# Kernel tuning notes

Measured on AMD Instinct MI355X. Metric: run time of the kernel, lower is better.

Reference implementation:

```python
import jax, jax.numpy as jnp
import numpy as np

NEG = -1e30  # safe -inf surrogate for log-space DP
BLANK = 0    # torch.nn.CTCLoss default blank index


def _ctc_loss_sum(lp, labels, in_lens, lab_lens):
    """CTC negative log-likelihood, summed over batch.
    lp: [T, B, V] log-probabilities; labels: [B, L] int; in_lens, lab_lens: [B] int.
    """
    T, B, V = lp.shape
    L = labels.shape[1]
    S = 2 * L + 1  # extended label length (blanks interleaved)
    s = jnp.arange(S)
    # extended label sequence z: blank at even positions, label at odd
    ext = jnp.where(s % 2 == 0, BLANK, labels[:, jnp.clip((s - 1) // 2, 0, L - 1)])  # [B,S]
    ext_m2 = jnp.concatenate([jnp.full((B, 2), BLANK, ext.dtype), ext[:, :-2]], axis=1)
    skip = (s >= 2) & (ext != BLANK) & (ext != ext_m2)  # [B,S] skip-transition allowed
    # emission log-probs gathered at extended labels: [T,B,S]
    emit = jnp.take_along_axis(lp, jnp.broadcast_to(ext[None], (T, B, S)), axis=2)
    alpha0 = jnp.full((B, S), NEG, lp.dtype)
    alpha0 = alpha0.at[:, 0].set(emit[0, :, 0]).at[:, 1].set(emit[0, :, 1])

    def step(alpha, inputs):
        emit_t, t = inputs
        a1 = jnp.concatenate([jnp.full((B, 1), NEG, alpha.dtype), alpha[:, :-1]], axis=1)
        a2 = jnp.concatenate([jnp.full((B, 2), NEG, alpha.dtype), alpha[:, :-2]], axis=1)
        comb = jnp.logaddexp(alpha, a1)
        comb = jnp.where(skip, jnp.logaddexp(comb, a2), comb)
        new = comb + emit_t
        # past each sequence's length, freeze alpha
        new = jnp.where(t < in_lens[:, None], new, alpha)
        return new, None

    alpha, _ = jax.lax.scan(step, alpha0, (emit[1:], jnp.arange(1, T)))
    s_last = 2 * lab_lens  # final blank position per sample
    bidx = jnp.arange(B)
    ll = jnp.logaddexp(alpha[bidx, s_last], alpha[bidx, s_last - 1])
    return jnp.sum(-ll)


def setup_inputs() -> dict:
    key = jax.random.key(0)
    k1, k2, k3, k4, k5, k6 = jax.random.split(key, 6)
    B, T, H, V, L = 16, 512, 512, 4096, 64
    hs_pad = jax.random.normal(k1, (B, T, H), dtype=jnp.float32)
    hs_lens = jax.random.randint(k2, (B,), T // 2, T + 1, dtype=jnp.int32)
    ys_pad = jax.random.randint(k3, (B, L), 1, V, dtype=jnp.int32)  # avoid blank=0
    ys_lens = jax.random.randint(k4, (B,), L // 2, L + 1, dtype=jnp.int32)
    W = jax.random.normal(k5, (H, V), dtype=jnp.float32) * (H ** -0.5)
    b = jax.random.normal(k6, (V,), dtype=jnp.float32) * 0.01
    return {"hs_pad": hs_pad, "hs_lens": hs_lens, "ys_pad": ys_pad,
            "ys_lens": ys_lens, "W": W, "b": b}


def reference(hs_pad, hs_lens, ys_pad, ys_lens, W, b):
    # projection (dropout_rate=0.0 -> identity) + log_softmax
    logits = jnp.einsum('bth,hv->btv', hs_pad, W) + b
    log_probs = jax.nn.log_softmax(logits, axis=-1)
    lp = jnp.transpose(log_probs, (1, 0, 2))  # [T,B,V]
    B = lp.shape[1]
    loss = _ctc_loss_sum(lp, ys_pad, hs_lens, ys_lens)
    return loss / B
```

## Files before the change

kernel.cpp:

```cpp
#include <hip/hip_runtime.h>
#include <hip/hip_bf16.h>
#include <math.h>

#define BB   16
#define TT   512
#define HH   512
#define VV   4096
#define LL   64
#define SS   129
#define JJ   65
#define MM   (BB*TT)

#define LOG2E 1.4426950408889634f
#define LN2   0.6931471805599453f

typedef __bf16 bf16;
typedef __attribute__((ext_vector_type(4))) __bf16 bf16x4;
typedef __attribute__((ext_vector_type(8))) __bf16 bf16x8;
typedef __attribute__((ext_vector_type(4))) float f32x4;

__global__ __launch_bounds__(256) void conv_hs(const float* __restrict__ hs,
                                               bf16* __restrict__ Abf)
{
    int idx = blockIdx.x * blockDim.x + threadIdx.x;
    const int n4 = MM * HH / 4;
    if (idx >= n4) return;
    float4 v = ((const float4*)hs)[idx];
    bf16x4 o = {(bf16)v.x, (bf16)v.y, (bf16)v.z, (bf16)v.w};
    *(bf16x4*)(Abf + (size_t)idx * 4) = o;
}

__global__ __launch_bounds__(256) void transpose_w(const float* __restrict__ W,
                                                   bf16* __restrict__ Wt)
{
    __shared__ float t[64][65];
    const int n0 = blockIdx.x * 64;
    const int k0 = blockIdx.y * 64;
    const int tid = threadIdx.x;
    #pragma unroll
    for (int i = 0; i < 16; ++i) {
        int idx = tid + i * 256;
        int kk = idx >> 6, nn = idx & 63;
        t[kk][nn] = W[(size_t)(k0 + kk) * VV + n0 + nn];
    }
    __syncthreads();
    #pragma unroll
    for (int i = 0; i < 16; ++i) {
        int idx = tid + i * 256;
        int nl = idx >> 6, kk = idx & 63;
        Wt[(size_t)(n0 + nl) * HH + k0 + kk] = (bf16)t[kk][nl];
    }
}

__global__ void make_cmap(const int* __restrict__ ys, int* __restrict__ cmap)
{
    int idx = threadIdx.x + blockIdx.x * blockDim.x;
    if (idx >= BB * JJ) return;
    int b = idx / JJ, j = idx % JJ;
    cmap[idx] = (j == 0) ? 0 : ys[b * LL + j - 1];
}

#define TN 128
#define NT64 (VV / 64)

#define GLDS(src, dst) \
    __builtin_amdgcn_global_load_lds((const __attribute__((address_space(1))) void*)(src), \
                                     (__attribute__((address_space(3))) void*)(dst), 16, 0, 0)

__global__ __launch_bounds__(256) void gemm_lse_mfma(
    const bf16* __restrict__ A,
    const bf16* __restrict__ Bt,
    const float* __restrict__ bias,
    const int*  __restrict__ cmap,
    float* __restrict__ part,
    float* __restrict__ glp_raw)
{
    __shared__ bf16 As[128 * 32];
    __shared__ bf16 Bs[128 * 32];
    const int tid = threadIdx.x;
    const int lane = tid & 63;
    const int wid = tid >> 6;
    const int wm = wid >> 1, wn = wid & 1;
    const int m0 = blockIdx.y * 128, n0 = blockIdx.x * 128;
    const int lq = lane & 15, kg = lane >> 4;

    f32x4 acc[4][4];
    const f32x4 z = {0.f, 0.f, 0.f, 0.f};
    #pragma unroll
    for (int i = 0; i < 4; ++i)
        #pragma unroll
        for (int j = 0; j < 4; ++j) acc[i][j] = z;

    const int c0 = tid;
    const int row0 = c0 >> 2, sl0 = (c0 & 3) ^ (row0 & 3);
    const int c1 = tid + 256;
    const int row1 = c1 >> 2, sl1 = (c1 & 3) ^ (row1 & 3);
    bf16* dstA0 = As + (size_t)(0 * 256 + (tid & 192)) * 8;
    bf16* dstA1 = As + (size_t)(1 * 256 + (tid & 192)) * 8;
    bf16* dstB0 = Bs + (size_t)(0 * 256 + (tid & 192)) * 8;
    bf16* dstB1 = Bs + (size_t)(1 * 256 + (tid & 192)) * 8;
    const bf16* srcA0 = A  + (size_t)(m0 + row0) * HH + sl0 * 8;
    const bf16* srcA1 = A  + (size_t)(m0 + row1) * HH + sl1 * 8;
    const bf16* srcB0 = Bt + (size_t)(n0 + row0) * HH + sl0 * 8;
    const bf16* srcB1 = Bt + (size_t)(n0 + row1) * HH + sl1 * 8;

    for (int k0 = 0; k0 < HH; k0 += 32) {
        GLDS(srcA0 + k0, dstA0);
        GLDS(srcA1 + k0, dstA1);
        GLDS(srcB0 + k0, dstB0);
        GLDS(srcB1 + k0, dstB1);
        __syncthreads();
        bf16x8 a[4], b[4];
        #pragma unroll
        for (int i = 0; i < 4; ++i) {
            int ar = wm * 64 + i * 16 + lq;
            a[i] = *(const bf16x8*)&As[ar * 32 + ((kg ^ (ar & 3)) * 8)];
        }
        #pragma unroll
        for (int j = 0; j < 4; ++j) {
            int br = wn * 64 + j * 16 + lq;
            b[j] = *(const bf16x8*)&Bs[br * 32 + ((kg ^ (br & 3)) * 8)];
        }
        #pragma unroll
        for (int i = 0; i < 4; ++i)
            #pragma unroll
            for (int j = 0; j < 4; ++j)
                acc[i][j] = __builtin_amdgcn_mfma_f32_16x16x32_bf16(a[i], b[j], acc[i][j], 0, 0, 0);
        __syncthreads();
    }

    const int ct = blockIdx.x * 2 + wn;
    float bj[4];
    #pragma unroll
    for (int j = 0; j < 4; ++j) bj[j] = bias[n0 + wn * 64 + j * 16 + lq];
    #pragma unroll
    for (int i = 0; i < 4; ++i) {
        #pragma unroll
        for (int r = 0; r < 4; ++r) {
            float v[4], mx = -3.4e38f;
            #pragma unroll
            for (int j = 0; j < 4; ++j) { v[j] = acc[i][j][r] + bj[j]; mx = fmaxf(mx, v[j]); }
            #pragma unroll
            for (int d = 1; d < 16; d <<= 1) mx = fmaxf(mx, __shfl_xor(mx, d));
            float sm = 0.f;
            #pragma unroll
            for (int j = 0; j < 4; ++j) sm += __expf(v[j] - mx);
            #pragma unroll
            for (int d = 1; d < 16; d <<= 1) sm += __shfl_xor(sm, d);
            if (lq == 0) {
                int rowg = m0 + wm * 64 + i * 16 + kg * 4 + r;
                size_t o = ((size_t)rowg * NT64 + ct) * 2;
                part[o] = mx; part[o + 1] = sm;
            }
        }
    }

    const int bidx  = m0 >> 9;
    const int nbase = n0 + wn * 64;
    for (int j = 0; j < JJ; ++j) {
        int c = cmap[bidx * JJ + j];
        int local = c - nbase;
        if (local >= 0 && local < 64) {
            int cl = local & 15;
            float bc = bias[c];
            #pragma unroll
            for (int jt = 0; jt < 4; ++jt) {
                if ((local >> 4) == jt && lq == cl) {
                    #pragma unroll
                    for (int i = 0; i < 4; ++i)
                        #pragma unroll
                        for (int r = 0; r < 4; ++r) {
                            int m = m0 + wm * 64 + i * 16 + kg * 4 + r;
                            glp_raw[(size_t)m * JJ + j] = acc[i][jt][r] + bc;
                        }
                }
            }
        }
    }
}

__global__ void lse_merge(const float* __restrict__ part, float* __restrict__ lse)
{
    int r = blockIdx.x * blockDim.x + threadIdx.x;
    if (r >= MM) return;
    const float* p = part + (size_t)r * NT64 * 2;
    float mx = -3.4e38f;
    #pragma unroll 4
    for (int nt = 0; nt < NT64; ++nt) mx = fmaxf(mx, p[2 * nt]);
    float s = 0.f;
    #pragma unroll 4
    for (int nt = 0; nt < NT64; ++nt) s += p[2 * nt + 1] * __expf(p[2 * nt] - mx);
    lse[r] = mx + logf(s);
}

__device__ __forceinline__ float dpp_shr1_zero(float x) {
    int r = __builtin_amdgcn_update_dpp(0, __float_as_int(x),
                                        0x138 , 0xF, 0xF, false);
    return __int_as_float(r);
}
template<int CTRL>
__device__ __forceinline__ float dpp_max_t(float m) {
    int r = __builtin_amdgcn_update_dpp(0, __float_as_int(m), CTRL, 0xF, 0xF, false);
    return fmaxf(m, __int_as_float(r));
}

#define LOADR(rv, gv, tbase) \
    _Pragma("unroll") \
    for (int u = 0; u < 16; ++u) { \
        int tt = (tbase) + u; tt = tt < TT ? tt : (TT - 1); \
        float raw0 = g[tt * JJ]; \
        float rawB = g[tt * JJ + l + 1]; \
        rv[u] = __builtin_amdgcn_exp2f((rawB - raw0) * LOG2E); \
        gv[u] = (raw0 - ls[tt]) * LOG2E; \
    }

#define RESCALE() { \
        float m_ = fmaxf(fmaxf(vA ? A : 0.f, vB ? B : 0.f), vC ? C : 0.f); \
        m_ = dpp_max_t<0x111>(m_);  \
        m_ = dpp_max_t<0x112>(m_);  \
        m_ = dpp_max_t<0x114>(m_);  \
        m_ = dpp_max_t<0x118>(m_);  \
        m_ = dpp_max_t<0x142>(m_);  \
        m_ = dpp_max_t<0x143>(m_);  \
        int mb = __builtin_amdgcn_readlane(__float_as_int(m_), 63); \
        int k_ = ((mb >> 23) & 0xFF) - 127; \
        float sc = __int_as_float((127 - k_) << 23); \
        A *= sc; B *= sc; C *= sc; K += k_; \
    }

#define DOCHUNK(rv, gv, tbase) { \
    const int tb_ = (tbase); \
    if (tb_ + 16 <= Tin) { \
        _Pragma("unroll") \
        for (int u = 0; u < 16; ++u) { \
            float prevB = dpp_shr1_zero(B); \
            float nA = A + prevB; \
            float t1 = A + B; \
            float t2 = skipB ? prevB : 0.f; \
            float nB = (t1 + t2) * rv[u]; \
            float nC = C + B; \
            A = nA; B = nB; C = nC; corr += gv[u]; \
            if (u == 7 || u == 15) RESCALE(); \
        } \
    } else { \
        _Pragma("unroll") \
        for (int u = 0; u < 16; ++u) { \
            bool upd = (tb_ + u) < Tin; \
            float prevB = dpp_shr1_zero(B); \
            float nA = A + prevB; \
            float t1 = A + B; \
            float t2 = skipB ? prevB : 0.f; \
            float nB = (t1 + t2) * rv[u]; \
            float nC = C + B; \
            A = upd ? nA : A; B = upd ? nB : B; C = upd ? nC : C; \
            corr += upd ? gv[u] : 0.f; \
            if (u == 7 || u == 15) RESCALE(); \
        } \
    } }

__global__ __launch_bounds__(64) void ctc_dp(
    const float* __restrict__ glp_raw, const float* __restrict__ lse,
    const int* __restrict__ ys, const int* __restrict__ hs_lens,
    const int* __restrict__ ys_lens, float* __restrict__ nll)
{
    const int b = blockIdx.x;
    const int l = threadIdx.x;
    const float* g  = glp_raw + (size_t)b * TT * JJ;
    const float* ls = lse + (size_t)b * TT;
    const int Tin = hs_lens[b];
    const int Ll  = ys_lens[b];

    const bool vA = (l <= Ll);
    const bool vB = (l <  Ll);
    const bool vC = (l == 63) && (Ll == 64);

    int cc = ys[b * LL + l];
    bool skipB = false;
    if (l >= 1) { int cp = ys[b * LL + l - 1]; skipB = (cc != 0) && (cc != cp); }

    float raw0_0 = g[0];
    float d0 = (g[l + 1] - raw0_0) * LOG2E;
    float A = (l == 0) ? 1.0f : 0.0f;
    float B = (l == 0) ? __builtin_amdgcn_exp2f(d0) : 0.0f;
    float C = 0.0f;
    float corr = (raw0_0 - ls[0]) * LOG2E;
    int K = 0;

    float ra[16], ga_[16], rb[16], gb_[16];
    LOADR(ra, ga_, 1);
    for (int tc = 1; tc < Tin; tc += 32) {
        LOADR(rb, gb_, tc + 16);
        DOCHUNK(ra, ga_, tc);
        LOADR(ra, ga_, tc + 32);
        if (tc + 16 < Tin) DOCHUNK(rb, gb_, tc + 16);
    }

    float v1 = (Ll == 64) ? __shfl(C, 63, 64) : __shfl(A, Ll, 64);
    float v2 = __shfl(B, Ll - 1, 64);
    if (l == 0) {
        float ll2 = __builtin_amdgcn_logf(v1 + v2) + (float)K + corr;
        nll[b] = -ll2 * LN2;
    }
}

__global__ void finalize(const float* __restrict__ nll, float* __restrict__ out)
{
    float v = (threadIdx.x < BB) ? nll[threadIdx.x] : 0.f;
    #pragma unroll
    for (int d = 32; d >= 1; d >>= 1) v += __shfl_down(v, d);
    if (threadIdx.x == 0) out[0] = v / (float)BB;
}

extern "C" void kernel_launch(void* const* d_in, const int* in_sizes, int n_in,
                              void* d_out, int out_size, void* d_ws, size_t ws_size,
                              hipStream_t stream) {
    const float* hs      = (const float*)d_in[0];
    const int*   hs_lens = (const int*)  d_in[1];
    const int*   ys      = (const int*)  d_in[2];
    const int*   ys_lens = (const int*)  d_in[3];
    const float* W       = (const float*)d_in[4];
    const float* bias    = (const float*)d_in[5];
    float* out = (float*)d_out;

    float* ws      = (float*)d_ws;
    float* part    = ws;
    float* lse     = part + (size_t)MM * NT64 * 2;
    float* glp_raw = lse  + MM;
    float* nll     = glp_raw + (size_t)MM * JJ;
    int*   cmap    = (int*)(nll + 16);
    bf16*  Abf     = (bf16*)(cmap + 1040);
    bf16*  Wt      = Abf + (size_t)MM * HH;

    conv_hs<<<(MM * HH / 4 + 255) / 256, 256, 0, stream>>>(hs, Abf);
    transpose_w<<<dim3(VV / 64, HH / 64), 256, 0, stream>>>(W, Wt);
    make_cmap<<<(BB * JJ + 255) / 256, 256, 0, stream>>>(ys, cmap);
    gemm_lse_mfma<<<dim3(VV / TN, MM / 128), 256, 0, stream>>>(Abf, Wt, bias, cmap, part, glp_raw);
    lse_merge<<<(MM + 255) / 256, 256, 0, stream>>>(part, lse);
    ctc_dp<<<BB, 64, 0, stream>>>(glp_raw, lse, ys, hs_lens, ys_lens, nll);
    finalize<<<1, 64, 0, stream>>>(nll, out);
}
```

Before: 207.7 us.

## Transpose gathered emissions to time-major rows, fuse prep kernels, wave-parallel LSE merge

Several changes land together. The GEMM epilogue now writes the gathered label logits as [B][J][T], so the serial CTC DP can fetch 16 timesteps per label with float4 loads instead of strided scalar loads. The per-step log-sum-exp correction is pulled out of the DP loop and summed once with a wave reduction. The hs conversion, the W transpose and the cmap kernels are merged into one prep launch, with cmap replaced by direct ys reads. lse_merge changes from one thread per row to one wave per row using shuffle reductions. The cost is a more involved block indexing in the DP, including skipping t=0 in the first block.

```diff
diff --git a/kernel.cpp b/kernel.cpp
--- a/kernel.cpp
+++ b/kernel.cpp
@@ -19,45 +19,37 @@
 typedef __attribute__((ext_vector_type(8))) __bf16 bf16x8;
 typedef __attribute__((ext_vector_type(4))) float f32x4;
 
-__global__ __launch_bounds__(256) void conv_hs(const float* __restrict__ hs,
-                                               bf16* __restrict__ Abf)
-{
-    int idx = blockIdx.x * blockDim.x + threadIdx.x;
-    const int n4 = MM * HH / 4;
-    if (idx >= n4) return;
-    float4 v = ((const float4*)hs)[idx];
-    bf16x4 o = {(bf16)v.x, (bf16)v.y, (bf16)v.z, (bf16)v.w};
-    *(bf16x4*)(Abf + (size_t)idx * 4) = o;
-}
-
-__global__ __launch_bounds__(256) void transpose_w(const float* __restrict__ W,
-                                                   bf16* __restrict__ Wt)
+__global__ __launch_bounds__(256) void prep(const float* __restrict__ hs,
+                                            const float* __restrict__ W,
+                                            bf16* __restrict__ Abf,
+                                            bf16* __restrict__ Wt)
 {
     __shared__ float t[64][65];
-    const int n0 = blockIdx.x * 64;
-    const int k0 = blockIdx.y * 64;
     const int tid = threadIdx.x;
-    #pragma unroll
-    for (int i = 0; i < 16; ++i) {
-        int idx = tid + i * 256;
-        int kk = idx >> 6, nn = idx & 63;
-        t[kk][nn] = W[(size_t)(k0 + kk) * VV + n0 + nn];
-    }
-    __syncthreads();
-    #pragma unroll
-    for (int i = 0; i < 16; ++i) {
-        int idx = tid + i * 256;
-        int nl = idx >> 6, kk = idx & 63;
-        Wt[(size_t)(n0 + nl) * HH + k0 + kk] = (bf16)t[kk][nl];
-    }
-}
-
-__global__ void make_cmap(const int* __restrict__ ys, int* __restrict__ cmap)
-{
-    int idx = threadIdx.x + blockIdx.x * blockDim.x;
-    if (idx >= BB * JJ) return;
-    int b = idx / JJ, j = idx % JJ;
-    cmap[idx] = (j == 0) ? 0 : ys[b * LL + j - 1];
+    int bx = blockIdx.x;
+    if (bx < 4096) {
+        int idx = bx * 256 + tid;
+        float4 v = ((const float4*)hs)[idx];
+        bf16x4 o = {(bf16)v.x, (bf16)v.y, (bf16)v.z, (bf16)v.w};
+        *(bf16x4*)(Abf + (size_t)idx * 4) = o;
+    } else {
+        bx -= 4096;
+        const int n0 = (bx & 63) * 64;
+        const int k0 = (bx >> 6) * 64;
+        #pragma unroll
+        for (int i = 0; i < 16; ++i) {
+            int idx = tid + i * 256;
+            int kk = idx >> 6, nn = idx & 63;
+            t[kk][nn] = W[(size_t)(k0 + kk) * VV + n0 + nn];
+        }
+        __syncthreads();
+        #pragma unroll
+        for (int i = 0; i < 16; ++i) {
+            int idx = tid + i * 256;
+            int nl = idx >> 6, kk = idx & 63;
+            Wt[(size_t)(n0 + nl) * HH + k0 + kk] = (bf16)t[kk][nl];
+        }
+    }
 }
 
 #define TN 128
@@ -71,9 +63,9 @@
     const bf16* __restrict__ A,
     const bf16* __restrict__ Bt,
     const float* __restrict__ bias,
-    const int*  __restrict__ cmap,
+    const int*  __restrict__ ys,
     float* __restrict__ part,
-    float* __restrict__ glp_raw)
+    float* __restrict__ glpT)
 {
     __shared__ bf16 As[128 * 32];
     __shared__ bf16 Bs[128 * 32];
@@ -155,10 +147,11 @@
         }
     }
 
-    const int bidx  = m0 >> 9;
+    const int bidx = m0 >> 9;
+    const int t0s  = (m0 & 511) + wm * 64;
     const int nbase = n0 + wn * 64;
     for (int j = 0; j < JJ; ++j) {
-        int c = cmap[bidx * JJ + j];
+        int c = (j == 0) ? 0 : ys[bidx * LL + j - 1];
         int local = c - nbase;
         if (local >= 0 && local < 64) {
             int cl = local & 15;
@@ -166,31 +159,34 @@
             #pragma unroll
             for (int jt = 0; jt < 4; ++jt) {
                 if ((local >> 4) == jt && lq == cl) {
+                    float* dst = glpT + ((size_t)(bidx * JJ + j)) * TT + t0s + kg * 4;
                     #pragma unroll
-                    for (int i = 0; i < 4; ++i)
-                        #pragma unroll
-                        for (int r = 0; r < 4; ++r) {
-                            int m = m0 + wm * 64 + i * 16 + kg * 4 + r;
-                            glp_raw[(size_t)m * JJ + j] = acc[i][jt][r] + bc;
-                        }
+                    for (int i = 0; i < 4; ++i) {
+                        f32x4 sv = acc[i][jt];
+                        float4 o4 = {sv[0] + bc, sv[1] + bc, sv[2] + bc, sv[3] + bc};
+                        *(float4*)(dst + i * 16) = o4;
+                    }
                 }
             }
         }
     }
 }
 
-__global__ void lse_merge(const float* __restrict__ part, float* __restrict__ lse)
-{
-    int r = blockIdx.x * blockDim.x + threadIdx.x;
-    if (r >= MM) return;
-    const float* p = part + (size_t)r * NT64 * 2;
-    float mx = -3.4e38f;
-    #pragma unroll 4
-    for (int nt = 0; nt < NT64; ++nt) mx = fmaxf(mx, p[2 * nt]);
-    float s = 0.f;
-    #pragma unroll 4
-    for (int nt = 0; nt < NT64; ++nt) s += p[2 * nt + 1] * __expf(p[2 * nt] - mx);
-    lse[r] = mx + logf(s);
+__global__ __launch_bounds__(256) void lse_merge(const float* __restrict__ part,
+                                                 float* __restrict__ lse)
+{
+    const int lane = threadIdx.x & 63;
+    const int r = blockIdx.x * 4 + (threadIdx.x >> 6);
+    const float* p = part + (size_t)r * (NT64 * 2);
+    float mx = p[2 * lane];
+    float sm = p[2 * lane + 1];
+    float wmax = mx;
+    #pragma unroll
+    for (int d = 1; d < 64; d <<= 1) wmax = fmaxf(wmax, __shfl_xor(wmax, d));
+    float c = sm * __expf(mx - wmax);
+    #pragma unroll
+    for (int d = 1; d < 64; d <<= 1) c += __shfl_xor(c, d);
+    if (lane == 0) lse[r] = wmax + logf(c);
 }
 
 __device__ __forceinline__ float dpp_shr1_zero(float x) {
@@ -204,15 +200,20 @@
     return fmaxf(m, __int_as_float(r));
 }
 
-#define LOADR(rv, gv, tbase) \
+#define LOADA(rv, gv, blk) { \
+    int bb_ = (blk); bb_ = bb_ < 32 ? bb_ : 31; \
+    const float4* p0_ = (const float4*)(g0 + bb_ * 16); \
+    const float4* pB_ = (const float4*)(gB + bb_ * 16); \
+    float4 q0_[4], qB_[4]; \
+    q0_[0] = p0_[0]; q0_[1] = p0_[1]; q0_[2] = p0_[2]; q0_[3] = p0_[3]; \
+    qB_[0] = pB_[0]; qB_[1] = pB_[1]; qB_[2] = pB_[2]; qB_[3] = pB_[3]; \
     _Pragma("unroll") \
     for (int u = 0; u < 16; ++u) { \
-        int tt = (tbase) + u; tt = tt < TT ? tt : (TT - 1); \
-        float raw0 = g[tt * JJ]; \
-        float rawB = g[tt * JJ + l + 1]; \
-        rv[u] = __builtin_amdgcn_exp2f((rawB - raw0) * LOG2E); \
-        gv[u] = (raw0 - ls[tt]) * LOG2E; \
-    }
+        float raw0_ = ((const float*)q0_)[u]; \
+        float rawB_ = ((const float*)qB_)[u]; \
+        rv[u] = __builtin_amdgcn_exp2f((rawB_ - raw0_) * LOG2E); \
+        gv[u] = raw0_; \
+    } }
 
 #define RESCALE() { \
         float m_ = fmaxf(fmaxf(vA ? A : 0.f, vB ? B : 0.f), vC ? C : 0.f); \
@@ -228,9 +229,9 @@
         A *= sc; B *= sc; C *= sc; K += k_; \
     }
 
-#define DOCHUNK(rv, gv, tbase) { \
-    const int tb_ = (tbase); \
-    if (tb_ + 16 <= Tin) { \
+#define DO16(rv, gv, blk, SKIP0) { \
+    const int tB_ = (blk) * 16; \
+    if (!(SKIP0) && tB_ + 16 <= Tin) { \
         _Pragma("unroll") \
         for (int u = 0; u < 16; ++u) { \
             float prevB = dpp_shr1_zero(B); \
@@ -245,7 +246,8 @@
     } else { \
         _Pragma("unroll") \
         for (int u = 0; u < 16; ++u) { \
-            bool upd = (tb_ + u) < Tin; \
+            int t_ = tB_ + u; \
+            bool upd = (t_ >= 1) && (t_ < Tin); \
             float prevB = dpp_shr1_zero(B); \
             float nA = A + prevB; \
             float t1 = A + B; \
@@ -259,13 +261,14 @@
     } }
 
 __global__ __launch_bounds__(64) void ctc_dp(
-    const float* __restrict__ glp_raw, const float* __restrict__ lse,
+    const float* __restrict__ glpT, const float* __restrict__ lse,
     const int* __restrict__ ys, const int* __restrict__ hs_lens,
     const int* __restrict__ ys_lens, float* __restrict__ nll)
 {
     const int b = blockIdx.x;
     const int l = threadIdx.x;
-    const float* g  = glp_raw + (size_t)b * TT * JJ;
+    const float* g0 = glpT + (size_t)(b * JJ) * TT;
+    const float* gB = glpT + (size_t)(b * JJ + l + 1) * TT;
     const float* ls = lse + (size_t)b * TT;
     const int Tin = hs_lens[b];
     const int Ll  = ys_lens[b];
@@ -278,27 +281,33 @@
     bool skipB = false;
     if (l >= 1) { int cp = ys[b * LL + l - 1]; skipB = (cc != 0) && (cc != cp); }
 
-    float raw0_0 = g[0];
-    float d0 = (g[l + 1] - raw0_0) * LOG2E;
+    float raw0_0 = g0[0];
+    float d0 = (gB[0] - raw0_0) * LOG2E;
     float A = (l == 0) ? 1.0f : 0.0f;
     float B = (l == 0) ? __builtin_amdgcn_exp2f(d0) : 0.0f;
     float C = 0.0f;
-    float corr = (raw0_0 - ls[0]) * LOG2E;
+    float corr = raw0_0;
     int K = 0;
 
-    float ra[16], ga_[16], rb[16], gb_[16];
-    LOADR(ra, ga_, 1);
-    for (int tc = 1; tc < Tin; tc += 32) {
-        LOADR(rb, gb_, tc + 16);
-        DOCHUNK(ra, ga_, tc);
-        LOADR(ra, ga_, tc + 32);
-        if (tc + 16 < Tin) DOCHUNK(rb, gb_, tc + 16);
-    }
+    float ra[16], ga[16], rb[16], gb[16];
+    LOADA(ra, ga, 0);
+    for (int blk = 0; blk < 32; blk += 2) {
+        LOADA(rb, gb, blk + 1);
+        DO16(ra, ga, blk, (blk == 0));
+        LOADA(ra, ga, blk + 2);
+        DO16(rb, gb, blk + 1, false);
+        if (16 * (blk + 2) >= Tin) break;
+    }
+
+    float lsum = 0.f;
+    for (int tt = l; tt < Tin; tt += 64) lsum += ls[tt];
+    #pragma unroll
+    for (int d = 1; d < 64; d <<= 1) lsum += __shfl_xor(lsum, d);
 
     float v1 = (Ll == 64) ? __shfl(C, 63, 64) : __shfl(A, Ll, 64);
     float v2 = __shfl(B, Ll - 1, 64);
     if (l == 0) {
-        float ll2 = __builtin_amdgcn_logf(v1 + v2) + (float)K + corr;
+        float ll2 = __builtin_amdgcn_logf(v1 + v2) + (float)K + (corr - lsum) * LOG2E;
         nll[b] = -ll2 * LN2;
     }
 }
@@ -322,20 +331,17 @@
     const float* bias    = (const float*)d_in[5];
     float* out = (float*)d_out;
 
-    float* ws      = (float*)d_ws;
-    float* part    = ws;
-    float* lse     = part + (size_t)MM * NT64 * 2;
-    float* glp_raw = lse  + MM;
-    float* nll     = glp_raw + (size_t)MM * JJ;
-    int*   cmap    = (int*)(nll + 16);
-    bf16*  Abf     = (bf16*)(cmap + 1040);
-    bf16*  Wt      = Abf + (size_t)MM * HH;
-
-    conv_hs<<<(MM * HH / 4 + 255) / 256, 256, 0, stream>>>(hs, Abf);
-    transpose_w<<<dim3(VV / 64, HH / 64), 256, 0, stream>>>(W, Wt);
-    make_cmap<<<(BB * JJ + 255) / 256, 256, 0, stream>>>(ys, cmap);
-    gemm_lse_mfma<<<dim3(VV / TN, MM / 128), 256, 0, stream>>>(Abf, Wt, bias, cmap, part, glp_raw);
-    lse_merge<<<(MM + 255) / 256, 256, 0, stream>>>(part, lse);
-    ctc_dp<<<BB, 64, 0, stream>>>(glp_raw, lse, ys, hs_lens, ys_lens, nll);
+    float* ws   = (float*)d_ws;
+    float* part = ws;
+    float* lse  = part + (size_t)MM * NT64 * 2;
+    float* glpT = lse  + MM;
+    float* nll  = glpT + (size_t)BB * JJ * TT;
+    bf16*  Abf  = (bf16*)(nll + 16);
+    bf16*  Wt   = Abf + (size_t)MM * HH;
+
+    prep<<<4608, 256, 0, stream>>>(hs, W, Abf, Wt);
+    gemm_lse_mfma<<<dim3(VV / TN, MM / 128), 256, 0, stream>>>(Abf, Wt, bias, ys, part, glpT);
+    lse_merge<<<MM / 4, 256, 0, stream>>>(part, lse);
+    ctc_dp<<<BB, 64, 0, stream>>>(glpT, lse, ys, hs_lens, ys_lens, nll);
     finalize<<<1, 64, 0, stream>>>(nll, out);
 }
```

After: 199.8 us. 1.04x faster.
